# Optimization experiments

Measured on AMD Instinct MI355X. Metric: run time of the kernel, lower is better.

## Reference

```python
import jax, jax.numpy as jnp
import numpy as np
import math

N_NODES = 50000
N_EDGES = 800000
F_IN = 32
HID = 64


def _layernorm(x, g, b, eps=1e-5):
    mu = x.mean(-1, keepdims=True)
    var = ((x - mu) ** 2).mean(-1, keepdims=True)
    return (x - mu) / jnp.sqrt(var + eps) * g + b


def _tconv(x, src, dst, Wq, bq, Wk, bk, Wv, bv, Ws, heads):
    # PyG TransformerConv (concat=True, root_weight=True, bias=False on skip)
    N = x.shape[0]
    C = Wq.shape[1] // heads
    q = (x @ Wq + bq).reshape(N, heads, C)[dst]  # [E,H,C] gathered at targets
    k = (x @ Wk + bk).reshape(N, heads, C)[src]  # [E,H,C] gathered at sources
    v = (x @ Wv + bv).reshape(N, heads, C)[src]
    scores = (q * k).sum(-1) / math.sqrt(C)      # [E,H]
    m = jax.ops.segment_max(scores, dst, num_segments=N)   # [N,H]
    p = jnp.exp(scores - m[dst])
    denom = jax.ops.segment_sum(p, dst, num_segments=N)
    alpha = p / (denom[dst] + 1e-16)             # segment softmax over in-edges
    agg = jax.ops.segment_sum(v * alpha[..., None], dst, num_segments=N)
    return agg.reshape(N, heads * C) + x @ Ws    # + skip (no bias)


def setup_inputs() -> dict:
    key = jax.random.key(0)
    ks = iter(jax.random.split(key, 64))
    def rn(shape, s=0.1):
        return jax.random.normal(next(ks), shape, jnp.float32) * s
    inp = {
        "x": rn((N_NODES, F_IN), 1.0),
        "edge_index": jax.random.randint(next(ks), (2, N_EDGES), 0, N_NODES, dtype=jnp.int32),
        "ln0_g": jnp.ones((F_IN,), jnp.float32),
        "ln0_b": jnp.zeros((F_IN,), jnp.float32),
    }
    dims = [F_IN, HID, HID]
    for l in range(3):
        d = dims[l]
        inp[f"Wq{l}"] = rn((d, HID)); inp[f"bq{l}"] = rn((HID,), 0.05)
        inp[f"Wk{l}"] = rn((d, HID)); inp[f"bk{l}"] = rn((HID,), 0.05)
        inp[f"Wv{l}"] = rn((d, HID)); inp[f"bv{l}"] = rn((HID,), 0.05)
        inp[f"Ws{l}"] = rn((d, HID))
        inp[f"g{l}"] = jnp.ones((HID,), jnp.float32)
        inp[f"b{l}"] = jnp.zeros((HID,), jnp.float32)
    inp["Wr1"] = rn((HID, HID // 2)); inp["br1"] = jnp.zeros((HID // 2,), jnp.float32)
    inp["Wr2"] = rn((HID // 2, 1));   inp["br2"] = jnp.zeros((1,), jnp.float32)
    inp["Wt1"] = rn((HID, HID // 2)); inp["bt1"] = jnp.zeros((HID // 2,), jnp.float32)
    inp["Wt2"] = rn((HID // 2, 1));   inp["bt2"] = jnp.zeros((1,), jnp.float32)
    return inp


def reference(x, edge_index, ln0_g, ln0_b,
              Wq0, bq0, Wk0, bk0, Wv0, bv0, Ws0, g0, b0,
              Wq1, bq1, Wk1, bk1, Wv1, bv1, Ws1, g1, b1,
              Wq2, bq2, Wk2, bk2, Wv2, bv2, Ws2, g2, b2,
              Wr1, br1, Wr2, br2, Wt1, bt1, Wt2, bt2):
    src, dst = edge_index[0], edge_index[1]
    h = _layernorm(x, ln0_g, ln0_b)
    layers = [
        (Wq0, bq0, Wk0, bk0, Wv0, bv0, Ws0, g0, b0, 4),
        (Wq1, bq1, Wk1, bk1, Wv1, bv1, Ws1, g1, b1, 4),
        (Wq2, bq2, Wk2, bk2, Wv2, bv2, Ws2, g2, b2, 1),
    ]
    for i, (Wq, bq, Wk, bk, Wv, bv, Ws, g, b, heads) in enumerate(layers):
        x_res = h if h.shape[-1] == HID else None
        h = _tconv(h, src, dst, Wq, bq, Wk, bk, Wv, bv, Ws, heads)
        h = _layernorm(h, g, b)
        if x_res is not None and i > 0:
            h = h + 0.1 * x_res
        if i < len(layers) - 1:
            h = jax.nn.relu(h)  # dropout is identity in eval mode
    rtt = jax.nn.relu(h @ Wr1 + br1) @ Wr2 + br2      # [N,1]
    retrans = jax.nn.relu(h @ Wt1 + bt1) @ Wt2 + bt2  # [N,1]
    return jnp.concatenate([rtt, retrans], axis=1)    # [N,2]
```

## Files before the change

kernel.cpp:

```cpp
#include <hip/hip_runtime.h>
#include <hip/hip_bf16.h>
#include <math.h>

#define N_NODES 50000
#define N_EDGES 800000
#define HID 64
#define NBK 196
#define EPB 1024
#define SB  782
#define FLAT (NBK * SB)
#define SCAN_B ((FLAT + 255) / 256)

#define LN0_BLKS   6250
#define HIST_BLKS  SB
#define WP0_BLKS   32
#define WP12_BLKS  64
#define PREP_BLKS  (LN0_BLKS + HIST_BLKS + WP0_BLKS + 2 * WP12_BLKS)

typedef __attribute__((ext_vector_type(8))) short short8;
typedef __attribute__((ext_vector_type(4))) float float4v;

__device__ __forceinline__ unsigned short f32_to_bf16_rne(float f) {
    unsigned int u = __float_as_uint(f);
    unsigned int r = u + 0x7fffu + ((u >> 16) & 1u);
    return (unsigned short)(r >> 16);
}

__device__ __forceinline__ void ln0_body(int b, int t,
        const float* __restrict__ x, const float* __restrict__ g,
        const float* __restrict__ bb, float* __restrict__ h0) {
    int lane = t & 63;
    int n = b * 8 + (t >> 6) * 2 + (lane >> 5);
    int c = lane & 31;
    float v = x[n * 32 + c];
    float s = v;
    #pragma unroll
    for (int off = 1; off < 32; off <<= 1) s += __shfl_xor(s, off);
    float mu = s * (1.0f / 32.0f);
    float d = v - mu;
    float vs = d * d;
    #pragma unroll
    for (int off = 1; off < 32; off <<= 1) vs += __shfl_xor(vs, off);
    float var = vs * (1.0f / 32.0f);
    h0[n * 32 + c] = d * rsqrtf(var + 1e-5f) * g[c] + bb[c];
}

__device__ __forceinline__ void wprep_body(int idx, int KS,
        const float* __restrict__ Wq, const float* __restrict__ Wk,
        const float* __restrict__ Wv, const float* __restrict__ Ws,
        unsigned short* __restrict__ Wp) {
    int j = idx & 7;
    int lane = (idx >> 3) & 63;
    int ts = idx >> 9;
    int s = ts % KS;
    int tile = ts / KS;
    int which = tile >> 2;
    int slice = tile & 3;
    int k = s * 32 + ((lane >> 4) * 8) + j;
    int col = slice * 16 + (lane & 15);
    const float* W = (which == 0) ? Wq : (which == 1) ? Wk : (which == 2) ? Wv : Ws;
    Wp[idx] = f32_to_bf16_rne(W[k * 64 + col]);
}

__global__ __launch_bounds__(256) void prep_kernel(
        const float* __restrict__ x, const float* __restrict__ ln0g,
        const float* __restrict__ ln0b, float* __restrict__ h0,
        const int* __restrict__ dst, int* __restrict__ ghist,
        const float* __restrict__ Wq0, const float* __restrict__ Wk0,
        const float* __restrict__ Wv0, const float* __restrict__ Ws0,
        unsigned short* __restrict__ Wp0,
        const float* __restrict__ Wq1, const float* __restrict__ Wk1,
        const float* __restrict__ Wv1, const float* __restrict__ Ws1,
        unsigned short* __restrict__ Wp1,
        const float* __restrict__ Wq2, const float* __restrict__ Wk2,
        const float* __restrict__ Wv2, const float* __restrict__ Ws2,
        unsigned short* __restrict__ Wp2) {
    __shared__ int hist[NBK];
    int b = blockIdx.x;
    int t = threadIdx.x;
    if (b < LN0_BLKS) {
        ln0_body(b, t, x, ln0g, ln0b, h0);
    } else if (b < LN0_BLKS + HIST_BLKS) {
        int i = b - LN0_BLKS;
        for (int k = t; k < NBK; k += 256) hist[k] = 0;
        __syncthreads();
        int e0 = i * EPB;
        #pragma unroll
        for (int r = 0; r < 4; r++) {
            int e = e0 + r * 256 + t;
            if (e < N_EDGES) atomicAdd(&hist[dst[e] >> 8], 1);
        }
        __syncthreads();
        for (int k = t; k < NBK; k += 256) ghist[k * SB + i] = hist[k];
    } else if (b < LN0_BLKS + HIST_BLKS + WP0_BLKS) {
        int idx = (b - LN0_BLKS - HIST_BLKS) * 256 + t;
        wprep_body(idx, 1, Wq0, Wk0, Wv0, Ws0, Wp0);
    } else if (b < LN0_BLKS + HIST_BLKS + WP0_BLKS + WP12_BLKS) {
        int idx = (b - LN0_BLKS - HIST_BLKS - WP0_BLKS) * 256 + t;
        wprep_body(idx, 2, Wq1, Wk1, Wv1, Ws1, Wp1);
    } else {
        int idx = (b - LN0_BLKS - HIST_BLKS - WP0_BLKS - WP12_BLKS) * 256 + t;
        wprep_body(idx, 2, Wq2, Wk2, Wv2, Ws2, Wp2);
    }
}

__global__ void scan1_kernel(const int* __restrict__ ghist, int* __restrict__ csum) {
    int f = blockIdx.x * 256 + threadIdx.x;
    int v = (f < FLAT) ? ghist[f] : 0;
    #pragma unroll
    for (int off = 1; off < 64; off <<= 1) v += __shfl_xor(v, off);
    __shared__ int ws[4];
    if ((threadIdx.x & 63) == 0) ws[threadIdx.x >> 6] = v;
    __syncthreads();
    if (threadIdx.x == 0) csum[blockIdx.x] = ws[0] + ws[1] + ws[2] + ws[3];
}

__global__ void scan2_kernel(const int* __restrict__ csum, int* __restrict__ coff,
                             int* __restrict__ bbase, int* __restrict__ row_ptr) {
    int lane = threadIdx.x;
    int carry = 0;
    for (int base = 0; base < SCAN_B; base += 64) {
        int i = base + lane;
        int v = (i < SCAN_B) ? csum[i] : 0;
        int incl = v;
        #pragma unroll
        for (int off = 1; off < 64; off <<= 1) {
            int tt = __shfl_up(incl, off);
            if (lane >= off) incl += tt;
        }
        if (i < SCAN_B) coff[i] = carry + incl - v;
        carry += __shfl(incl, 63);
    }
    if (lane == 0) { bbase[NBK] = N_EDGES; row_ptr[N_NODES] = N_EDGES; }
}

__global__ void scan3_kernel(const int* __restrict__ ghist, const int* __restrict__ coff,
                             int* __restrict__ goff, int* __restrict__ bbase) {
    int f = blockIdx.x * 256 + threadIdx.x;
    int lane = threadIdx.x & 63;
    int w = threadIdx.x >> 6;
    int v = (f < FLAT) ? ghist[f] : 0;
    int incl = v;
    #pragma unroll
    for (int off = 1; off < 64; off <<= 1) {
        int tt = __shfl_up(incl, off);
        if (lane >= off) incl += tt;
    }
    __shared__ int ws[4];
    if (lane == 63) ws[w] = incl;
    __syncthreads();
    int woff = 0;
    #pragma unroll
    for (int k = 0; k < 4; k++) if (k < w) woff += ws[k];
    int excl = coff[blockIdx.x] + woff + incl - v;
    if (f < FLAT) {
        goff[f] = excl;
        if (f % SB == 0) bbase[f / SB] = excl;
    }
}

__global__ __launch_bounds__(256) void scatter_kernel(
        const int* __restrict__ src, const int* __restrict__ dst,
        const int* __restrict__ goff, int2* __restrict__ ebkt) {
    __shared__ int hist[NBK];
    int t = threadIdx.x, i = blockIdx.x;
    for (int k = t; k < NBK; k += 256) hist[k] = 0;
    __syncthreads();
    int e0 = i * EPB;
    #pragma unroll
    for (int r = 0; r < 4; r++) {
        int e = e0 + r * 256 + t;
        if (e < N_EDGES) {
            int s = src[e], d = dst[e];
            int k = d >> 8;
            int rank = atomicAdd(&hist[k], 1);
            ebkt[goff[k * SB + i] + rank] = make_int2(s, d);
        }
    }
}

__global__ __launch_bounds__(256) void bucket_build_kernel(
        const int2* __restrict__ ebkt, const int* __restrict__ bbase,
        int* __restrict__ row_ptr, int* __restrict__ colb) {
    __shared__ int ldeg[256];
    __shared__ int lcur[256];
    __shared__ int wsum[4];
    int b = blockIdx.x;
    int t = threadIdx.x;
    int cbase = bbase[b];
    int cnt = bbase[b + 1] - cbase;
    int ebase = cbase;

    ldeg[t] = 0;
    __syncthreads();
    for (int i = t; i < cnt; i += 256) {
        int2 e = ebkt[ebase + i];
        atomicAdd(&ldeg[e.y & 255], 1);
    }
    __syncthreads();

    int lane = t & 63;
    int w = t >> 6;
    int v = ldeg[t];
    int incl = v;
    #pragma unroll
    for (int off = 1; off < 64; off <<= 1) {
        int tt = __shfl_up(incl, off);
        if (lane >= off) incl += tt;
    }
    if (lane == 63) wsum[w] = incl;
    __syncthreads();
    int woff = 0;
    #pragma unroll
    for (int k = 0; k < 4; k++) if (k < w) woff += wsum[k];
    int excl = woff + incl - v;

    int node = b * 256 + t;
    if (node < N_NODES) row_ptr[node] = cbase + excl;
    lcur[t] = excl;
    __syncthreads();

    for (int i = t; i < cnt; i += 256) {
        int2 e = ebkt[ebase + i];
        int r = atomicAdd(&lcur[e.y & 255], 1);
        colb[cbase + r] = e.x;
    }
}

template <int D>
__global__ __launch_bounds__(256) void qkvs_mfma_kernel(
        const float* __restrict__ h,
        const unsigned short* __restrict__ Wp,
        const float* __restrict__ bq, const float* __restrict__ bk,
        const float* __restrict__ bv,
        float* __restrict__ Q, unsigned int* __restrict__ KV,
        float* __restrict__ S) {
    constexpr int KS = D / 32;
    int t = threadIdx.x;
    int lane = t & 63;
    int w = t >> 6;
    int n0 = blockIdx.x * 16;
    int n16 = lane & 15;
    int quad = lane >> 4;
    int col = w * 16 + n16;

    short8 afrag[KS];
    #pragma unroll
    for (int s = 0; s < KS; s++) {
        const float* hp = &h[(n0 + n16) * D + s * 32 + quad * 8];
        float4 a0 = *(const float4*)hp;
        float4 a1 = *(const float4*)(hp + 4);
        short8 af;
        af[0] = (short)f32_to_bf16_rne(a0.x);
        af[1] = (short)f32_to_bf16_rne(a0.y);
        af[2] = (short)f32_to_bf16_rne(a0.z);
        af[3] = (short)f32_to_bf16_rne(a0.w);
        af[4] = (short)f32_to_bf16_rne(a1.x);
        af[5] = (short)f32_to_bf16_rne(a1.y);
        af[6] = (short)f32_to_bf16_rne(a1.z);
        af[7] = (short)f32_to_bf16_rne(a1.w);
        afrag[s] = af;
    }

    float4v accs[4];
    #pragma unroll
    for (int which = 0; which < 4; which++) {
        float4v acc = {0.0f, 0.0f, 0.0f, 0.0f};
        int tile = which * 4 + w;
        #pragma unroll
        for (int s = 0; s < KS; s++) {
            short8 bfrag = *(const short8*)&Wp[((tile * KS + s) * 64 + lane) * 8];
            acc = __builtin_amdgcn_mfma_f32_16x16x32_bf16(afrag[s], bfrag, acc, 0, 0, 0);
        }
        accs[which] = acc;
    }

    float bqc = bq[col], bkc = bk[col], bvc = bv[col];

    #pragma unroll
    for (int r = 0; r < 4; r++) {
        int node = n0 + quad * 4 + r;
        Q[node * 64 + col] = accs[0][r] + bqc;
        unsigned int kw = f32_to_bf16_rne(accs[1][r] + bkc);
        unsigned int vw = f32_to_bf16_rne(accs[2][r] + bvc);
        KV[node * 64 + col] = (vw << 16) | kw;
        S[node * 64 + col] = accs[3][r];
    }
}

template <int HEADS, bool RES, bool RELU>
__global__ __launch_bounds__(256) void agg_kernel(
                           const float* __restrict__ Q, const unsigned int* __restrict__ KV,
                           const float* __restrict__ S,
                           const int* __restrict__ row_ptr, const int* __restrict__ colb,
                           const float* __restrict__ g, const float* __restrict__ b,
                           const float* __restrict__ h_in, float* __restrict__ h_out) {
    constexpr int C = HID / HEADS;
    int lane = threadIdx.x & 63;
    int m = lane & 15;
    int grp = lane >> 4;
    int n = blockIdx.x * 4 + (threadIdx.x >> 6);

    const float scale = rsqrtf((float)C);
    float4 q4 = *(const float4*)&Q[n * 64 + 4 * m];
    q4.x *= scale; q4.y *= scale; q4.z *= scale; q4.w *= scale;

    int beg = row_ptr[n], end = row_ptr[n + 1];

    float ssum = 0.0f;
    float acc0 = 0.0f, acc1 = 0.0f, acc2 = 0.0f, acc3 = 0.0f;

    for (int base = beg; base < end; base += 64) {
        int limit = min(end - base, 64);
        int src_l = (base + lane < end) ? colb[base + lane] : 0;
        for (int sub = 0; sub < limit; sub += 16) {
            int e0 = sub + grp, e1 = sub + 4 + grp, e2 = sub + 8 + grp, e3 = sub + 12 + grp;
            int s0 = __shfl(src_l, e0);
            int s1 = __shfl(src_l, e1);
            int s2 = __shfl(src_l, e2);
            int s3 = __shfl(src_l, e3);
            bool v0ok = e0 < limit, v1ok = e1 < limit, v2ok = e2 < limit, v3ok = e3 < limit;
            uint4 kv0 = make_uint4(0, 0, 0, 0), kv1 = kv0, kv2 = kv0, kv3 = kv0;
            if (v0ok) kv0 = *(const uint4*)&KV[(size_t)s0 * 64 + 4 * m];
            if (v1ok) kv1 = *(const uint4*)&KV[(size_t)s1 * 64 + 4 * m];
            if (v2ok) kv2 = *(const uint4*)&KV[(size_t)s2 * 64 + 4 * m];
            if (v3ok) kv3 = *(const uint4*)&KV[(size_t)s3 * 64 + 4 * m];

            float t0 = fmaf(q4.x, __uint_as_float(kv0.x << 16),
                       fmaf(q4.y, __uint_as_float(kv0.y << 16),
                       fmaf(q4.z, __uint_as_float(kv0.z << 16),
                            q4.w * __uint_as_float(kv0.w << 16))));
            float t1 = fmaf(q4.x, __uint_as_float(kv1.x << 16),
                       fmaf(q4.y, __uint_as_float(kv1.y << 16),
                       fmaf(q4.z, __uint_as_float(kv1.z << 16),
                            q4.w * __uint_as_float(kv1.w << 16))));
            float t2 = fmaf(q4.x, __uint_as_float(kv2.x << 16),
                       fmaf(q4.y, __uint_as_float(kv2.y << 16),
                       fmaf(q4.z, __uint_as_float(kv2.z << 16),
                            q4.w * __uint_as_float(kv2.w << 16))));
            float t3 = fmaf(q4.x, __uint_as_float(kv3.x << 16),
                       fmaf(q4.y, __uint_as_float(kv3.y << 16),
                       fmaf(q4.z, __uint_as_float(kv3.z << 16),
                            q4.w * __uint_as_float(kv3.w << 16))));
            #pragma unroll
            for (int off = 1; off < C / 4; off <<= 1) {
                t0 += __shfl_xor(t0, off);
                t1 += __shfl_xor(t1, off);
                t2 += __shfl_xor(t2, off);
                t3 += __shfl_xor(t3, off);
            }
            float p0 = v0ok ? __expf(t0) : 0.0f;
            float p1 = v1ok ? __expf(t1) : 0.0f;
            float p2 = v2ok ? __expf(t2) : 0.0f;
            float p3 = v3ok ? __expf(t3) : 0.0f;
            ssum += (p0 + p1) + (p2 + p3);
            acc0 = fmaf(p0, __uint_as_float(kv0.x & 0xffff0000u),
                   fmaf(p1, __uint_as_float(kv1.x & 0xffff0000u),
                   fmaf(p2, __uint_as_float(kv2.x & 0xffff0000u),
                   fmaf(p3, __uint_as_float(kv3.x & 0xffff0000u), acc0))));
            acc1 = fmaf(p0, __uint_as_float(kv0.y & 0xffff0000u),
                   fmaf(p1, __uint_as_float(kv1.y & 0xffff0000u),
                   fmaf(p2, __uint_as_float(kv2.y & 0xffff0000u),
                   fmaf(p3, __uint_as_float(kv3.y & 0xffff0000u), acc1))));
            acc2 = fmaf(p0, __uint_as_float(kv0.z & 0xffff0000u),
                   fmaf(p1, __uint_as_float(kv1.z & 0xffff0000u),
                   fmaf(p2, __uint_as_float(kv2.z & 0xffff0000u),
                   fmaf(p3, __uint_as_float(kv3.z & 0xffff0000u), acc2))));
            acc3 = fmaf(p0, __uint_as_float(kv0.w & 0xffff0000u),
                   fmaf(p1, __uint_as_float(kv1.w & 0xffff0000u),
                   fmaf(p2, __uint_as_float(kv2.w & 0xffff0000u),
                   fmaf(p3, __uint_as_float(kv3.w & 0xffff0000u), acc3))));
        }
    }

    #pragma unroll
    for (int off = 16; off < 64; off <<= 1) {
        ssum += __shfl_xor(ssum, off);
        acc0 += __shfl_xor(acc0, off);
        acc1 += __shfl_xor(acc1, off);
        acc2 += __shfl_xor(acc2, off);
        acc3 += __shfl_xor(acc3, off);
    }

    float inv = 1.0f / (ssum + 1e-16f);
    float4 sv = *(const float4*)&S[n * 64 + 4 * m];
    float o0 = fmaf(acc0, inv, sv.x);
    float o1 = fmaf(acc1, inv, sv.y);
    float o2 = fmaf(acc2, inv, sv.z);
    float o3 = fmaf(acc3, inv, sv.w);

    float s = (o0 + o1) + (o2 + o3);
    #pragma unroll
    for (int off = 1; off < 16; off <<= 1) s += __shfl_xor(s, off);
    float mu = s * (1.0f / 64.0f);
    float d0 = o0 - mu, d1 = o1 - mu, d2 = o2 - mu, d3 = o3 - mu;
    float vs = (d0 * d0 + d1 * d1) + (d2 * d2 + d3 * d3);
    #pragma unroll
    for (int off = 1; off < 16; off <<= 1) vs += __shfl_xor(vs, off);
    float rstd = rsqrtf(vs * (1.0f / 64.0f) + 1e-5f);

    float4 gv = *(const float4*)&g[4 * m];
    float4 bv = *(const float4*)&b[4 * m];
    float y0 = d0 * rstd * gv.x + bv.x;
    float y1 = d1 * rstd * gv.y + bv.y;
    float y2 = d2 * rstd * gv.z + bv.z;
    float y3 = d3 * rstd * gv.w + bv.w;
    if (RES) {
        float4 rv = *(const float4*)&h_in[n * 64 + 4 * m];
        y0 = fmaf(0.1f, rv.x, y0);
        y1 = fmaf(0.1f, rv.y, y1);
        y2 = fmaf(0.1f, rv.z, y2);
        y3 = fmaf(0.1f, rv.w, y3);
    }
    if (RELU) {
        y0 = fmaxf(y0, 0.0f); y1 = fmaxf(y1, 0.0f);
        y2 = fmaxf(y2, 0.0f); y3 = fmaxf(y3, 0.0f);
    }
    if (grp == 0) {
        float4 yv = make_float4(y0, y1, y2, y3);
        *(float4*)&h_out[n * 64 + 4 * m] = yv;
    }
}

__global__ void head_kernel(const float* __restrict__ h,
                            const float* __restrict__ Wr1, const float* __restrict__ br1,
                            const float* __restrict__ Wr2, const float* __restrict__ br2,
                            const float* __restrict__ Wt1, const float* __restrict__ bt1,
                            const float* __restrict__ Wt2, const float* __restrict__ bt2,
                            float* __restrict__ out) {
    __shared__ float sh[4][HID];
    int wave = threadIdx.x >> 6;
    int lane = threadIdx.x & 63;
    int n = blockIdx.x * 4 + wave;
    sh[wave][lane] = h[n * 64 + lane];
    __syncthreads();
    int half = lane >> 5;
    int j = lane & 31;
    const float* W1 = half ? Wt1 : Wr1;
    const float* b1 = half ? bt1 : br1;
    const float* W2 = half ? Wt2 : Wr2;
    const float* b2 = half ? bt2 : br2;
    float a = b1[j];
    #pragma unroll 8
    for (int i = 0; i < 64; i++) a = fmaf(sh[wave][i], W1[i * 32 + j], a);
    a = fmaxf(a, 0.0f);
    float r = a * W2[j];
    #pragma unroll
    for (int off = 1; off < 32; off <<= 1) r += __shfl_xor(r, off);
    if (j == 0) out[n * 2 + half] = r + b2[0];
}

extern "C" void kernel_launch(void* const* d_in, const int* in_sizes, int n_in,
                              void* d_out, int out_size, void* d_ws, size_t ws_size,
                              hipStream_t stream) {
    const float* x    = (const float*)d_in[0];
    const int*   ei   = (const int*)d_in[1];
    const int*   src  = ei;
    const int*   dst  = ei + N_EDGES;
    const float* ln0g = (const float*)d_in[2];
    const float* ln0b = (const float*)d_in[3];

    const float* P[27];
    for (int i = 0; i < 27; i++) P[i] = (const float*)d_in[4 + i];
    const float* Wr1 = (const float*)d_in[31];
    const float* br1 = (const float*)d_in[32];
    const float* Wr2 = (const float*)d_in[33];
    const float* br2 = (const float*)d_in[34];
    const float* Wt1 = (const float*)d_in[35];
    const float* bt1 = (const float*)d_in[36];
    const float* Wt2 = (const float*)d_in[37];
    const float* bt2 = (const float*)d_in[38];

    float* out = (float*)d_out;

    float* hbuf0 = (float*)d_ws;
    float* hbuf1 = hbuf0 + N_NODES * 64;
    float* Qb    = hbuf1 + N_NODES * 64;
    float* Sb    = Qb + N_NODES * 64;
    unsigned int* KVb = (unsigned int*)(Sb + N_NODES * 64);
    int* row_ptr = (int*)(KVb + N_NODES * 64);
    int* colb    = row_ptr + (N_NODES + 1);
    int* ghist   = colb + N_EDGES;
    int* goff    = ghist + FLAT;
    int* csum    = goff + FLAT;
    int* coff    = csum + SCAN_B;
    int* bbase   = coff + SCAN_B;
    unsigned short* Wp0 = (unsigned short*)(bbase + NBK + 1);
    unsigned short* Wp1 = Wp0 + 16 * 1 * 512;
    unsigned short* Wp2 = Wp1 + 16 * 2 * 512;
    int2* ebkt = (int2*)Qb;

    prep_kernel<<<PREP_BLKS, 256, 0, stream>>>(x, ln0g, ln0b, hbuf0,
        dst, ghist,
        P[0],  P[2],  P[4],  P[6],  Wp0,
        P[9],  P[11], P[13], P[15], Wp1,
        P[18], P[20], P[22], P[24], Wp2);
    scan1_kernel<<<SCAN_B, 256, 0, stream>>>(ghist, csum);
    scan2_kernel<<<1, 64, 0, stream>>>(csum, coff, bbase, row_ptr);
    scan3_kernel<<<SCAN_B, 256, 0, stream>>>(ghist, coff, goff, bbase);
    scatter_kernel<<<SB, 256, 0, stream>>>(src, dst, goff, ebkt);
    bucket_build_kernel<<<NBK, 256, 0, stream>>>(ebkt, bbase, row_ptr, colb);

    qkvs_mfma_kernel<32><<<3125, 256, 0, stream>>>(hbuf0, Wp0,
        P[1], P[3], P[5], Qb, KVb, Sb);
    agg_kernel<4, false, true><<<12500, 256, 0, stream>>>(Qb, KVb, Sb,
        row_ptr, colb, P[7], P[8], nullptr, hbuf1);

    qkvs_mfma_kernel<64><<<3125, 256, 0, stream>>>(hbuf1, Wp1,
        P[10], P[12], P[14], Qb, KVb, Sb);
    agg_kernel<4, true, true><<<12500, 256, 0, stream>>>(Qb, KVb, Sb,
        row_ptr, colb, P[16], P[17], hbuf1, hbuf0);

    qkvs_mfma_kernel<64><<<3125, 256, 0, stream>>>(hbuf0, Wp2,
        P[19], P[21], P[23], Qb, KVb, Sb);
    agg_kernel<1, true, false><<<12500, 256, 0, stream>>>(Qb, KVb, Sb,
        row_ptr, colb, P[25], P[26], hbuf0, hbuf1);

    head_kernel<<<12500, 256, 0, stream>>>(hbuf1,
        Wr1, br1, Wr2, br2, Wt1, bt1, Wt2, bt2, out);
}
```

Baseline: 349.3 us.

## Fuse CSR build into one cooperative kernel and fold head MLP into last aggregation

Merges the three scan kernels, the scatter and the bucket build into a single cooperative kernel that separates phases with grid-wide syncs. This removes five launches and their gaps. It also moves the output head MLP into the final aggregation kernel so the last hidden state goes through shared memory rather than a global round trip and another launch. The agg kernel gains a launch-bounds occupancy hint. The cost is that grid syncs serialize phases on a grid limited to resident blocks, and the head fusion adds a block barrier and extra registers to the last agg kernel.

```diff
diff --git a/kernel.cpp b/kernel.cpp
--- a/kernel.cpp
+++ b/kernel.cpp
@@ -1,6 +1,9 @@
 #include <hip/hip_runtime.h>
 #include <hip/hip_bf16.h>
+#include <hip/hip_cooperative_groups.h>
 #include <math.h>
+
+namespace cg = cooperative_groups;
 
 #define N_NODES 50000
 #define N_EDGES 800000
@@ -104,126 +107,126 @@
     }
 }
 
-__global__ void scan1_kernel(const int* __restrict__ ghist, int* __restrict__ csum) {
-    int f = blockIdx.x * 256 + threadIdx.x;
-    int v = (f < FLAT) ? ghist[f] : 0;
-    #pragma unroll
-    for (int off = 1; off < 64; off <<= 1) v += __shfl_xor(v, off);
+__global__ __launch_bounds__(256) void csr_kernel(
+        const int* __restrict__ src, const int* __restrict__ dst,
+        const int* __restrict__ ghist,
+        int* __restrict__ csum, int* __restrict__ coff,
+        int* __restrict__ goff, int* __restrict__ bbase,
+        int* __restrict__ row_ptr, int* __restrict__ colb,
+        int2* __restrict__ ebkt) {
+    cg::grid_group grid = cg::this_grid();
     __shared__ int ws[4];
-    if ((threadIdx.x & 63) == 0) ws[threadIdx.x >> 6] = v;
-    __syncthreads();
-    if (threadIdx.x == 0) csum[blockIdx.x] = ws[0] + ws[1] + ws[2] + ws[3];
-}
-
-__global__ void scan2_kernel(const int* __restrict__ csum, int* __restrict__ coff,
-                             int* __restrict__ bbase, int* __restrict__ row_ptr) {
-    int lane = threadIdx.x;
-    int carry = 0;
-    for (int base = 0; base < SCAN_B; base += 64) {
-        int i = base + lane;
-        int v = (i < SCAN_B) ? csum[i] : 0;
+    __shared__ int hist[NBK];
+    __shared__ int ldeg[256];
+    __shared__ int lcur[256];
+    int t = threadIdx.x;
+    int lane = t & 63;
+    int w = t >> 6;
+
+    for (int vb = blockIdx.x; vb < SCAN_B; vb += gridDim.x) {
+        int f = vb * 256 + t;
+        int v = (f < FLAT) ? ghist[f] : 0;
+        #pragma unroll
+        for (int off = 1; off < 64; off <<= 1) v += __shfl_xor(v, off);
+        if (lane == 0) ws[w] = v;
+        __syncthreads();
+        if (t == 0) csum[vb] = ws[0] + ws[1] + ws[2] + ws[3];
+        __syncthreads();
+    }
+    grid.sync();
+
+    if (blockIdx.x == 0 && t < 64) {
+        int carry = 0;
+        for (int base = 0; base < SCAN_B; base += 64) {
+            int i = base + lane;
+            int v = (i < SCAN_B) ? csum[i] : 0;
+            int incl = v;
+            #pragma unroll
+            for (int off = 1; off < 64; off <<= 1) {
+                int tt = __shfl_up(incl, off);
+                if (lane >= off) incl += tt;
+            }
+            if (i < SCAN_B) coff[i] = carry + incl - v;
+            carry += __shfl(incl, 63);
+        }
+        if (lane == 0) { bbase[NBK] = N_EDGES; row_ptr[N_NODES] = N_EDGES; }
+    }
+    grid.sync();
+
+    for (int vb = blockIdx.x; vb < SCAN_B; vb += gridDim.x) {
+        int f = vb * 256 + t;
+        int v = (f < FLAT) ? ghist[f] : 0;
         int incl = v;
         #pragma unroll
         for (int off = 1; off < 64; off <<= 1) {
             int tt = __shfl_up(incl, off);
             if (lane >= off) incl += tt;
         }
-        if (i < SCAN_B) coff[i] = carry + incl - v;
-        carry += __shfl(incl, 63);
-    }
-    if (lane == 0) { bbase[NBK] = N_EDGES; row_ptr[N_NODES] = N_EDGES; }
-}
-
-__global__ void scan3_kernel(const int* __restrict__ ghist, const int* __restrict__ coff,
-                             int* __restrict__ goff, int* __restrict__ bbase) {
-    int f = blockIdx.x * 256 + threadIdx.x;
-    int lane = threadIdx.x & 63;
-    int w = threadIdx.x >> 6;
-    int v = (f < FLAT) ? ghist[f] : 0;
-    int incl = v;
-    #pragma unroll
-    for (int off = 1; off < 64; off <<= 1) {
-        int tt = __shfl_up(incl, off);
-        if (lane >= off) incl += tt;
-    }
-    __shared__ int ws[4];
-    if (lane == 63) ws[w] = incl;
-    __syncthreads();
-    int woff = 0;
-    #pragma unroll
-    for (int k = 0; k < 4; k++) if (k < w) woff += ws[k];
-    int excl = coff[blockIdx.x] + woff + incl - v;
-    if (f < FLAT) {
-        goff[f] = excl;
-        if (f % SB == 0) bbase[f / SB] = excl;
-    }
-}
-
-__global__ __launch_bounds__(256) void scatter_kernel(
-        const int* __restrict__ src, const int* __restrict__ dst,
-        const int* __restrict__ goff, int2* __restrict__ ebkt) {
-    __shared__ int hist[NBK];
-    int t = threadIdx.x, i = blockIdx.x;
-    for (int k = t; k < NBK; k += 256) hist[k] = 0;
-    __syncthreads();
-    int e0 = i * EPB;
-    #pragma unroll
-    for (int r = 0; r < 4; r++) {
-        int e = e0 + r * 256 + t;
-        if (e < N_EDGES) {
-            int s = src[e], d = dst[e];
-            int k = d >> 8;
-            int rank = atomicAdd(&hist[k], 1);
-            ebkt[goff[k * SB + i] + rank] = make_int2(s, d);
-        }
-    }
-}
-
-__global__ __launch_bounds__(256) void bucket_build_kernel(
-        const int2* __restrict__ ebkt, const int* __restrict__ bbase,
-        int* __restrict__ row_ptr, int* __restrict__ colb) {
-    __shared__ int ldeg[256];
-    __shared__ int lcur[256];
-    __shared__ int wsum[4];
-    int b = blockIdx.x;
-    int t = threadIdx.x;
-    int cbase = bbase[b];
-    int cnt = bbase[b + 1] - cbase;
-    int ebase = cbase;
-
-    ldeg[t] = 0;
-    __syncthreads();
-    for (int i = t; i < cnt; i += 256) {
-        int2 e = ebkt[ebase + i];
-        atomicAdd(&ldeg[e.y & 255], 1);
-    }
-    __syncthreads();
-
-    int lane = t & 63;
-    int w = t >> 6;
-    int v = ldeg[t];
-    int incl = v;
-    #pragma unroll
-    for (int off = 1; off < 64; off <<= 1) {
-        int tt = __shfl_up(incl, off);
-        if (lane >= off) incl += tt;
-    }
-    if (lane == 63) wsum[w] = incl;
-    __syncthreads();
-    int woff = 0;
-    #pragma unroll
-    for (int k = 0; k < 4; k++) if (k < w) woff += wsum[k];
-    int excl = woff + incl - v;
-
-    int node = b * 256 + t;
-    if (node < N_NODES) row_ptr[node] = cbase + excl;
-    lcur[t] = excl;
-    __syncthreads();
-
-    for (int i = t; i < cnt; i += 256) {
-        int2 e = ebkt[ebase + i];
-        int r = atomicAdd(&lcur[e.y & 255], 1);
-        colb[cbase + r] = e.x;
+        if (lane == 63) ws[w] = incl;
+        __syncthreads();
+        int woff = 0;
+        #pragma unroll
+        for (int k = 0; k < 4; k++) if (k < w) woff += ws[k];
+        int excl = coff[vb] + woff + incl - v;
+        if (f < FLAT) {
+            goff[f] = excl;
+            if (f % SB == 0) bbase[f / SB] = excl;
+        }
+        __syncthreads();
+    }
+    grid.sync();
+
+    for (int vb = blockIdx.x; vb < SB; vb += gridDim.x) {
+        for (int k = t; k < NBK; k += 256) hist[k] = 0;
+        __syncthreads();
+        int e0 = vb * EPB;
+        #pragma unroll
+        for (int r = 0; r < 4; r++) {
+            int e = e0 + r * 256 + t;
+            if (e < N_EDGES) {
+                int s = src[e], d = dst[e];
+                int k = d >> 8;
+                int rank = atomicAdd(&hist[k], 1);
+                ebkt[goff[k * SB + vb] + rank] = make_int2(s, d);
+            }
+        }
+        __syncthreads();
+    }
+    grid.sync();
+
+    for (int vb = blockIdx.x; vb < NBK; vb += gridDim.x) {
+        int cbase = bbase[vb];
+        int cnt = bbase[vb + 1] - cbase;
+        ldeg[t] = 0;
+        __syncthreads();
+        for (int i = t; i < cnt; i += 256) {
+            int2 e = ebkt[cbase + i];
+            atomicAdd(&ldeg[e.y & 255], 1);
+        }
+        __syncthreads();
+        int v = ldeg[t];
+        int incl = v;
+        #pragma unroll
+        for (int off = 1; off < 64; off <<= 1) {
+            int tt = __shfl_up(incl, off);
+            if (lane >= off) incl += tt;
+        }
+        if (lane == 63) ws[w] = incl;
+        __syncthreads();
+        int woff = 0;
+        #pragma unroll
+        for (int k = 0; k < 4; k++) if (k < w) woff += ws[k];
+        int excl = woff + incl - v;
+        int node = vb * 256 + t;
+        if (node < N_NODES) row_ptr[node] = cbase + excl;
+        lcur[t] = excl;
+        __syncthreads();
+        for (int i = t; i < cnt; i += 256) {
+            int2 e = ebkt[cbase + i];
+            int r = atomicAdd(&lcur[e.y & 255], 1);
+            colb[cbase + r] = e.x;
+        }
+        __syncthreads();
     }
 }
 
@@ -288,13 +291,18 @@
     }
 }
 
-template <int HEADS, bool RES, bool RELU>
-__global__ __launch_bounds__(256) void agg_kernel(
+template <int HEADS, bool RES, bool RELU, bool HEAD>
+__global__ __launch_bounds__(256, 8) void agg_kernel(
                            const float* __restrict__ Q, const unsigned int* __restrict__ KV,
                            const float* __restrict__ S,
                            const int* __restrict__ row_ptr, const int* __restrict__ colb,
                            const float* __restrict__ g, const float* __restrict__ b,
-                           const float* __restrict__ h_in, float* __restrict__ h_out) {
+                           const float* __restrict__ h_in, float* __restrict__ h_out,
+                           const float* __restrict__ Wr1, const float* __restrict__ br1,
+                           const float* __restrict__ Wr2, const float* __restrict__ br2,
+                           const float* __restrict__ Wt1, const float* __restrict__ bt1,
+                           const float* __restrict__ Wt2, const float* __restrict__ bt2,
+                           float* __restrict__ out) {
     constexpr int C = HID / HEADS;
     int lane = threadIdx.x & 63;
     int m = lane & 15;
@@ -416,38 +424,35 @@
         y0 = fmaxf(y0, 0.0f); y1 = fmaxf(y1, 0.0f);
         y2 = fmaxf(y2, 0.0f); y3 = fmaxf(y3, 0.0f);
     }
-    if (grp == 0) {
-        float4 yv = make_float4(y0, y1, y2, y3);
-        *(float4*)&h_out[n * 64 + 4 * m] = yv;
-    }
-}
-
-__global__ void head_kernel(const float* __restrict__ h,
-                            const float* __restrict__ Wr1, const float* __restrict__ br1,
-                            const float* __restrict__ Wr2, const float* __restrict__ br2,
-                            const float* __restrict__ Wt1, const float* __restrict__ bt1,
-                            const float* __restrict__ Wt2, const float* __restrict__ bt2,
-                            float* __restrict__ out) {
-    __shared__ float sh[4][HID];
-    int wave = threadIdx.x >> 6;
-    int lane = threadIdx.x & 63;
-    int n = blockIdx.x * 4 + wave;
-    sh[wave][lane] = h[n * 64 + lane];
-    __syncthreads();
-    int half = lane >> 5;
-    int j = lane & 31;
-    const float* W1 = half ? Wt1 : Wr1;
-    const float* b1 = half ? bt1 : br1;
-    const float* W2 = half ? Wt2 : Wr2;
-    const float* b2 = half ? bt2 : br2;
-    float a = b1[j];
-    #pragma unroll 8
-    for (int i = 0; i < 64; i++) a = fmaf(sh[wave][i], W1[i * 32 + j], a);
-    a = fmaxf(a, 0.0f);
-    float r = a * W2[j];
-    #pragma unroll
-    for (int off = 1; off < 32; off <<= 1) r += __shfl_xor(r, off);
-    if (j == 0) out[n * 2 + half] = r + b2[0];
+
+    if (!HEAD) {
+        if (grp == 0) {
+            float4 yv = make_float4(y0, y1, y2, y3);
+            *(float4*)&h_out[n * 64 + 4 * m] = yv;
+        }
+    } else {
+        __shared__ float sh[4][HID];
+        int wave = threadIdx.x >> 6;
+        if (grp == 0) {
+            float4 yv = make_float4(y0, y1, y2, y3);
+            *(float4*)&sh[wave][4 * m] = yv;
+        }
+        __syncthreads();
+        int half = lane >> 5;
+        int j = lane & 31;
+        const float* W1 = half ? Wt1 : Wr1;
+        const float* b1 = half ? bt1 : br1;
+        const float* W2 = half ? Wt2 : Wr2;
+        const float* b2v = half ? bt2 : br2;
+        float a = b1[j];
+        #pragma unroll 8
+        for (int i = 0; i < 64; i++) a = fmaf(sh[wave][i], W1[i * 32 + j], a);
+        a = fmaxf(a, 0.0f);
+        float r = a * W2[j];
+        #pragma unroll
+        for (int off = 1; off < 32; off <<= 1) r += __shfl_xor(r, off);
+        if (j == 0) out[n * 2 + half] = r + b2v[0];
+    }
 }
 
 extern "C" void kernel_launch(void* const* d_in, const int* in_sizes, int n_in,
@@ -495,27 +500,32 @@
         P[0],  P[2],  P[4],  P[6],  Wp0,
         P[9],  P[11], P[13], P[15], Wp1,
         P[18], P[20], P[22], P[24], Wp2);
-    scan1_kernel<<<SCAN_B, 256, 0, stream>>>(ghist, csum);
-    scan2_kernel<<<1, 64, 0, stream>>>(csum, coff, bbase, row_ptr);
-    scan3_kernel<<<SCAN_B, 256, 0, stream>>>(ghist, coff, goff, bbase);
-    scatter_kernel<<<SB, 256, 0, stream>>>(src, dst, goff, ebkt);
-    bucket_build_kernel<<<NBK, 256, 0, stream>>>(ebkt, bbase, row_ptr, colb);
+
+    int maxB = 0;
+    hipOccupancyMaxActiveBlocksPerMultiprocessor(&maxB, csr_kernel, 256, 0);
+    if (maxB < 1) maxB = 1;
+    int G = maxB * 256;
+    if (G > SB) G = SB;
+    void* cargs[] = {(void*)&src, (void*)&dst, (void*)&ghist, (void*)&csum,
+                     (void*)&coff, (void*)&goff, (void*)&bbase, (void*)&row_ptr,
+                     (void*)&colb, (void*)&ebkt};
+    hipLaunchCooperativeKernel((void*)csr_kernel, dim3(G), dim3(256), cargs, 0, stream);
 
     qkvs_mfma_kernel<32><<<3125, 256, 0, stream>>>(hbuf0, Wp0,
         P[1], P[3], P[5], Qb, KVb, Sb);
-    agg_kernel<4, false, true><<<12500, 256, 0, stream>>>(Qb, KVb, Sb,
-        row_ptr, colb, P[7], P[8], nullptr, hbuf1);
+    agg_kernel<4, false, true, false><<<12500, 256, 0, stream>>>(Qb, KVb, Sb,
+        row_ptr, colb, P[7], P[8], nullptr, hbuf1,
+        Wr1, br1, Wr2, br2, Wt1, bt1, Wt2, bt2, out);
 
     qkvs_mfma_kernel<64><<<3125, 256, 0, stream>>>(hbuf1, Wp1,
         P[10], P[12], P[14], Qb, KVb, Sb);
-    agg_kernel<4, true, true><<<12500, 256, 0, stream>>>(Qb, KVb, Sb,
-        row_ptr, colb, P[16], P[17], hbuf1, hbuf0);
+    agg_kernel<4, true, true, false><<<12500, 256, 0, stream>>>(Qb, KVb, Sb,
+        row_ptr, colb, P[16], P[17], hbuf1, hbuf0,
+        Wr1, br1, Wr2, br2, Wt1, bt1, Wt2, bt2, out);
 
     qkvs_mfma_kernel<64><<<3125, 256, 0, stream>>>(hbuf0, Wp2,
         P[19], P[21], P[23], Qb, KVb, Sb);
-    agg_kernel<1, true, false><<<12500, 256, 0, stream>>>(Qb, KVb, Sb,
-        row_ptr, colb, P[25], P[26], hbuf0, hbuf1);
-
-    head_kernel<<<12500, 256, 0, stream>>>(hbuf1,
+    agg_kernel<1, true, false, true><<<12500, 256, 0, stream>>>(Qb, KVb, Sb,
+        row_ptr, colb, P[25], P[26], hbuf0, hbuf1,
         Wr1, br1, Wr2, br2, Wt1, bt1, Wt2, bt2, out);
 }
```

Result: slower. 697.8 us (+99.8%).
